# Performance work log

Hardware: AMD Instinct MI355X
Metric: run time of the kernel (lower is better)

The kernel has to match this reference:

```python
import jax, jax.numpy as jnp
import numpy as np

B, T, TB, TV, TR = 4, 512, 512, 512, 256
D, H = 1024, 16
HD = D // H
D4 = D // 4
DFF = 4096
ROPE_THETA = 10000.0


def _rms(x, w, eps=1e-6):
    return x * jax.lax.rsqrt(jnp.mean(x * x, -1, keepdims=True) + eps) * w


def _ln(x, w, b, eps=1e-5):
    m = jnp.mean(x, -1, keepdims=True)
    v = jnp.var(x, -1, keepdims=True)
    return (x - m) * jax.lax.rsqrt(v + eps) * w + b


def _rope_cs(L, hd):
    inv = 1.0 / (ROPE_THETA ** (jnp.arange(0, hd, 2, dtype=jnp.float32) / hd))
    f = jnp.arange(L, dtype=jnp.float32)[:, None] * inv[None, :]
    e = jnp.concatenate([f, f], -1)  # (L, hd)
    return jnp.cos(e), jnp.sin(e)


def _rot_half(x):
    h = x.shape[-1] // 2
    return jnp.concatenate([-x[..., h:], x[..., :h]], -1)


def _rope(x, cos, sin):
    return x * cos + _rot_half(x) * sin


def _heads(x):
    b, l, _ = x.shape
    return x.reshape(b, l, H, HD).transpose(0, 2, 1, 3)  # (B,H,L,hd)


def setup_inputs() -> dict:
    key = jax.random.key(0)
    ks = jax.random.split(key, 16)
    def n(k, shape, s=0.02):
        return jax.random.normal(k, shape, jnp.float32) * s
    return {
        'x': n(ks[0], (B, T, D), 1.0),
        'bev_tokens': n(ks[1], (B, TB, D), 1.0),
        'vl_tokens': n(ks[2], (B, TV, D), 1.0),
        'reasoning_tokens': n(ks[3], (B, TR, D), 1.0),
        'conditioning': n(ks[4], (B, D), 1.0),
        'ln_pre_w': jnp.ones((D,)), 'ln_pre_b': jnp.zeros((D,)),
        'adaln_w': n(ks[5], (6 * D, D)), 'adaln_b': jnp.zeros((6 * D,)),
        'q_proj_w': n(ks[6], (D, D)), 'q_proj_b': jnp.zeros((D,)),
        'qa_w': n(ks[7], (3, D4, D)), 'qa_b': jnp.zeros((3, D4)),
        'qa_out_w': n(ks[8], (D, D4)), 'qa_out_b': jnp.zeros((D,)),
        'k_w': n(ks[9], (4, D, D)), 'k_b': jnp.zeros((4, D)),
        'v_w': n(ks[10], (4, D, D)), 'v_b': jnp.zeros((4, D)),
        'o_w': n(ks[11], (D, D)), 'o_b': jnp.zeros((D,)),
        'qn_w': jnp.ones((HD,)), 'kn_w': jnp.ones((HD,)),
        'gating': jnp.full((1,), 0.5, jnp.float32),
        'temps': jnp.zeros((4,)), 'score_biases': jnp.zeros((4,)),
        'ffn_ln_w': jnp.ones((D,)), 'ffn_ln_b': jnp.zeros((D,)),
        'ffn_w1': n(ks[12], (DFF, D)), 'ffn_b1': jnp.zeros((DFF,)),
        'ffn_w2': n(ks[13], (D, DFF)), 'ffn_b2': jnp.zeros((D,)),
    }


def reference(x, bev_tokens, vl_tokens, reasoning_tokens, conditioning,
              ln_pre_w, ln_pre_b, adaln_w, adaln_b,
              q_proj_w, q_proj_b, qa_w, qa_b, qa_out_w, qa_out_b,
              k_w, k_b, v_w, v_b, o_w, o_b, qn_w, kn_w,
              gating, temps, score_biases,
              ffn_ln_w, ffn_ln_b, ffn_w1, ffn_b1, ffn_w2, ffn_b2):
    # AdaLN modulation (T_route == 0 path: single modulation for whole sequence)
    mod = jax.nn.silu(conditioning) @ adaln_w.T + adaln_b  # (B, 6D)
    shift_pre, scale_pre, gate_attn, shift_ffn, scale_ffn, gate_ffn = jnp.split(mod, 6, axis=1)
    x_norm = _ln(x, ln_pre_w, ln_pre_b) * (1.0 + scale_pre[:, None, :]) + shift_pre[:, None, :]

    # Self Q and per-source K/V (sources: self, bev, vl, reasoning)
    q_self = _heads(x_norm @ q_proj_w.T + q_proj_b)
    srcs = [x_norm, bev_tokens, vl_tokens, reasoning_tokens]
    k_all = [_heads(s @ k_w[i].T + k_b[i]) for i, s in enumerate(srcs)]
    v_all = [_heads(s @ v_w[i].T + v_b[i]) for i, s in enumerate(srcs)]

    # Source-specific adapter queries: d -> d/4 -> d (shared out proj)
    q_ad = [_heads((x_norm @ qa_w[i].T + qa_b[i]) @ qa_out_w.T + qa_out_b) for i in range(3)]

    # QK-Norm (RMSNorm on head_dim)
    q_all = [_rms(q, qn_w) for q in [q_self] + q_ad]
    k_all = [_rms(k, kn_w) for k in k_all]

    # RoPE: Q and K for self-attention; K only for cross sources
    cosT, sinT = _rope_cs(x.shape[1], HD)
    q_all[0] = _rope(q_all[0], cosT, sinT)
    k_roped = []
    for k in k_all:
        c, s = _rope_cs(k.shape[2], HD)
        k_roped.append(_rope(k, c, s))

    # Per-source temperature / bias; gating only on reasoning scores
    temp = 1.0 + jax.nn.softplus(temps)
    ratio_g = jnp.tanh(gating[0])
    inv_sqrt_d = HD ** -0.5
    scores = []
    for i in range(4):
        s = jnp.einsum('bhqd,bhkd->bhqk', q_all[i], k_roped[i]) * (inv_sqrt_d * temp[i]) + score_biases[i]
        if i == 3:
            s = s * ratio_g
        scores.append(s)

    attn = jax.nn.softmax(jnp.concatenate(scores, -1), axis=-1)  # joint softmax
    v_cat = jnp.concatenate(v_all, 2)  # (B,H,T+TB+TV+TR,hd)
    out = jnp.einsum('bhqk,bhkd->bhqd', attn, v_cat)
    out = out.transpose(0, 2, 1, 3).reshape(x.shape) @ o_w.T + o_b
    x = x + gate_attn[:, None, :] * out

    # FFN with AdaLN modulation (dropout = identity at eval)
    h = _ln(x, ffn_ln_w, ffn_ln_b) * (1.0 + scale_ffn[:, None, :]) + shift_ffn[:, None, :]
    h = jax.nn.gelu(h @ ffn_w1.T + ffn_b1, approximate=False) @ ffn_w2.T + ffn_b2
    return x + gate_ffn[:, None, :] * h
```

## Files before the change

### kernel.cpp

```cpp
#include <hip/hip_runtime.h>

typedef unsigned short ushort_t;
typedef __attribute__((ext_vector_type(8))) __bf16 bf16x8;
typedef __attribute__((ext_vector_type(4))) float f32x4;

__device__ __forceinline__ float bf2f(ushort_t u) {
    union { unsigned int i; float f; } v; v.i = ((unsigned int)u) << 16; return v.f;
}
__device__ __forceinline__ ushort_t f2bf(float f) {
    union { float f; unsigned int i; } v; v.f = f;
    unsigned int r = (v.i + 0x7FFFu + ((v.i >> 16) & 1u)) >> 16;
    return (ushort_t)r;
}
__device__ __forceinline__ float gelu_exact(float v) {
    return 0.5f * v * (1.f + erff(v * 0.70710678118654752f));
}
__device__ __forceinline__ float ld1(const void* p, size_t i, int isf32) {
    return isf32 ? ((const float*)p)[i] : bf2f(((const ushort_t*)p)[i]);
}
__device__ __forceinline__ void stage8(const void* p, size_t idx, int isf32, ushort_t* dst) {
    if (isf32) {
        const float* f = (const float*)p + idx;
        float4 u = *(const float4*)f;
        float4 v = *(const float4*)(f + 4);
        dst[0] = f2bf(u.x); dst[1] = f2bf(u.y); dst[2] = f2bf(u.z); dst[3] = f2bf(u.w);
        dst[4] = f2bf(v.x); dst[5] = f2bf(v.y); dst[6] = f2bf(v.z); dst[7] = f2bf(v.w);
    } else {
        *(uint4*)dst = *(const uint4*)((const ushort_t*)p + idx);
    }
}
__device__ __forceinline__ void gload16(const ushort_t* g, ushort_t* l) {
    __builtin_amdgcn_global_load_lds(
        (const __attribute__((address_space(1))) unsigned int*)g,
        (__attribute__((address_space(3))) unsigned int*)l, 16, 0, 0);
}

__device__ __forceinline__ void store_q(ushort_t* qbuf, int row, int c, int p0, float v) {
    int b = row >> 9, t = row & 511;
    qbuf[((((size_t)(b * 16 + (c >> 6))) * 4 + p0) * 512 + t) * 64 + (c & 63)] = f2bf(v);
}
__device__ __forceinline__ void store_k(ushort_t* kbuf, int row, int c, int koff, int p1, float v) {
    int b = row >> p1, t = row & ((1 << p1) - 1);
    kbuf[(((size_t)(b * 16 + (c >> 6))) * 1792 + koff + t) * 64 + (c & 63)] = f2bf(v);
}
__device__ __forceinline__ void store_v(ushort_t* vbufT, int row, int c, int koff, int p1, float v) {
    int b = row >> p1, t = row & ((1 << p1) - 1);
    vbufT[(((size_t)(b * 16 + (c >> 6))) * 64 + (c & 63)) * 1792 + koff + t] = f2bf(v);
}

__global__ void detect_kernel(const unsigned int* __restrict__ x, int* __restrict__ flag) {
    if (threadIdx.x == 0 && blockIdx.x == 0) {
        int sane = 0;
        for (int i = 0; i < 256; i++) {
            unsigned int e = (x[i] >> 7) & 0xFFu;
            if (e == 0u || (e >= 100u && e <= 140u)) sane++;
        }
        *flag = (sane >= 200) ? 0 : 1;
    }
}

static constexpr size_t CW_QPROJ = 0;
static constexpr size_t CW_QA    = 1048576;
static constexpr size_t CW_QAOUT = 1835008;
static constexpr size_t CW_KW    = 2097152;
static constexpr size_t CW_VW    = 6291456;
static constexpr size_t CW_OW    = 10485760;
static constexpr size_t CW_FFN1  = 11534336;
static constexpr size_t CW_FFN2  = 15728640;
static constexpr size_t CW_TOTAL = 19922944;

__global__ void __launch_bounds__(256) convert_weights_kernel(
    const void* s0, const void* s1, const void* s2, const void* s3,
    const void* s4, const void* s5, const void* s6, const void* s7,
    ushort_t* __restrict__ dst, const int* __restrict__ dflag) {
    int isf32 = *dflag;
    size_t i8 = ((size_t)blockIdx.x * 256 + threadIdx.x) * 8;
    if (i8 >= CW_TOTAL) return;
    const void* src; size_t base;
    if      (i8 < CW_QA)    { src = s0; base = CW_QPROJ; }
    else if (i8 < CW_QAOUT) { src = s1; base = CW_QA; }
    else if (i8 < CW_KW)    { src = s2; base = CW_QAOUT; }
    else if (i8 < CW_VW)    { src = s3; base = CW_KW; }
    else if (i8 < CW_OW)    { src = s4; base = CW_VW; }
    else if (i8 < CW_FFN1)  { src = s5; base = CW_OW; }
    else if (i8 < CW_FFN2)  { src = s6; base = CW_FFN1; }
    else                    { src = s7; base = CW_FFN2; }
    ushort_t t8[8];
    stage8(src, i8 - base, isf32, t8);
    *(uint4*)(dst + i8) = *(uint4*)t8;
}

__global__ void __launch_bounds__(256) convert_act3_kernel(
    const void* __restrict__ bev, const void* __restrict__ vl,
    const void* __restrict__ reas, ushort_t* __restrict__ actA,
    ushort_t* __restrict__ actB, const int* __restrict__ dflag) {
    int isf32 = *dflag;
    size_t i8 = ((size_t)blockIdx.x * 256 + threadIdx.x) * 8;
    if (i8 >= 5242880) return;
    ushort_t t8[8];
    if (i8 < 2097152) {
        stage8(bev, i8, isf32, t8);
        *(uint4*)(actA + i8) = *(uint4*)t8;
    } else if (i8 < 4194304) {
        stage8(vl, i8 - 2097152, isf32, t8);
        *(uint4*)(actA + i8) = *(uint4*)t8;
    } else {
        stage8(reas, i8 - 4194304, isf32, t8);
        *(uint4*)(actB + (i8 - 4194304)) = *(uint4*)t8;
    }
}

__global__ void prep_consts_kernel(const void* __restrict__ temps,
                                   const void* __restrict__ biases,
                                   const void* __restrict__ gating,
                                   float* __restrict__ consts,
                                   const int* __restrict__ dflag) {
    if (threadIdx.x == 0 && blockIdx.x == 0) {
        int isf32 = *dflag;
        float g = tanhf(ld1(gating, 0, isf32));
        for (int s = 0; s < 4; s++) {
            float t  = ld1(temps, s, isf32);
            float sp = (t > 20.f) ? t : log1pf(expf(t));
            float scale = 0.125f * (1.f + sp);
            float mul = (s == 3) ? g : 1.f;
            consts[s]     = scale * mul;
            consts[4 + s] = ld1(biases, s, isf32) * mul;
        }
    }
}

__global__ void __launch_bounds__(256) adaln_kernel(
    const void* __restrict__ cond, const void* __restrict__ w,
    const void* __restrict__ bias, float* __restrict__ mod,
    int wmode, const int* __restrict__ dflag) {
    __shared__ float cs[1024];
    int isf32 = *dflag;
    int wf = (wmode == 2) ? 0 : isf32;
    int b = blockIdx.y, tid = threadIdx.x;
    for (int i = tid; i < 1024; i += 256) {
        float c = ld1(cond, b * 1024 + i, isf32);
        cs[i] = c / (1.f + expf(-c));
    }
    __syncthreads();
    int n = blockIdx.x * 256 + tid;
    float acc = 0.f;
    if (wf) {
        const float* wr = (const float*)w + (size_t)n * 1024;
        for (int d = 0; d < 1024; d += 8) {
            float4 a = *(const float4*)(wr + d);
            float4 bb = *(const float4*)(wr + d + 4);
            acc += cs[d+0]*a.x + cs[d+1]*a.y + cs[d+2]*a.z + cs[d+3]*a.w
                 + cs[d+4]*bb.x + cs[d+5]*bb.y + cs[d+6]*bb.z + cs[d+7]*bb.w;
        }
    } else {
        const ushort_t* wr = (const ushort_t*)w + (size_t)n * 1024;
        for (int d = 0; d < 1024; d += 8) {
            uint4 raw = *(const uint4*)(wr + d);
            const ushort_t* u = (const ushort_t*)&raw;
            acc += cs[d+0]*bf2f(u[0]) + cs[d+1]*bf2f(u[1]) + cs[d+2]*bf2f(u[2]) + cs[d+3]*bf2f(u[3])
                 + cs[d+4]*bf2f(u[4]) + cs[d+5]*bf2f(u[5]) + cs[d+6]*bf2f(u[6]) + cs[d+7]*bf2f(u[7]);
        }
    }
    mod[(size_t)b * 6144 + n] = acc + ld1(bias, n, isf32);
}

template <int SRC>
__global__ void __launch_bounds__(256) ln_mod_kernel(
    const void* __restrict__ xin, const float* __restrict__ mod,
    const void* __restrict__ lnw, const void* __restrict__ lnb,
    int shift_off, int scale_off, ushort_t* __restrict__ out,
    const int* __restrict__ dflag) {
    int isf32 = *dflag;
    int row = blockIdx.x, tid = threadIdx.x;
    int b = row >> 9;
    float v[4];
    #pragma unroll
    for (int i = 0; i < 4; i++) {
        size_t idx = (size_t)row * 1024 + tid + 256 * i;
        v[i] = (SRC == 1) ? ((const float*)xin)[idx] : ld1(xin, idx, isf32);
    }
    float s = v[0] + v[1] + v[2] + v[3];
    float ss = v[0]*v[0] + v[1]*v[1] + v[2]*v[2] + v[3]*v[3];
    #pragma unroll
    for (int off = 1; off < 64; off <<= 1) {
        s  += __shfl_xor(s,  off, 64);
        ss += __shfl_xor(ss, off, 64);
    }
    __shared__ float red[8];
    int w = tid >> 6;
    if ((tid & 63) == 0) { red[w] = s; red[4 + w] = ss; }
    __syncthreads();
    s  = red[0] + red[1] + red[2] + red[3];
    ss = red[4] + red[5] + red[6] + red[7];
    float mean = s * (1.f / 1024.f);
    float var  = ss * (1.f / 1024.f) - mean * mean;
    float inv  = rsqrtf(var + 1e-5f);
    const float* mb = mod + (size_t)b * 6144;
    #pragma unroll
    for (int i = 0; i < 4; i++) {
        int d = tid + 256 * i;
        float xn = (v[i] - mean) * inv;
        float y  = xn * ld1(lnw, d, isf32) + ld1(lnb, d, isf32);
        out[(size_t)row * 1024 + d] = f2bf(y * (1.f + mb[scale_off + d]) + mb[shift_off + d]);
    }
}

template <int EPI>
__global__ void __launch_bounds__(256) gemm_bt_kernel(
    const void* __restrict__ A, int lda,
    const void* __restrict__ W, int wrow0,
    const void* __restrict__ bias,
    void* __restrict__ Cout, int ldc, int K, int p0, int p1,
    int a_ext, int wmode, const int* __restrict__ dflag) {
    __shared__ ushort_t As[64][40];
    __shared__ ushort_t Bs[64][40];
    int isf32 = *dflag;
    int fa = a_ext ? isf32 : 0;
    int fw = (wmode == 2) ? 0 : isf32;
    int m0 = blockIdx.x * 64, n0 = blockIdx.y * 64;
    int tid = threadIdx.x;
    int r = tid >> 2, c = (tid & 3) * 8;
    int w = tid >> 6, ln = tid & 63;
    int msub = (w & 1) * 32, nsub = (w >> 1) * 32;
    int fr = ln & 15, q = ln >> 4;
    f32x4 acc00 = {0.f,0.f,0.f,0.f}, acc01 = {0.f,0.f,0.f,0.f};
    f32x4 acc10 = {0.f,0.f,0.f,0.f}, acc11 = {0.f,0.f,0.f,0.f};
    for (int k0 = 0; k0 < K; k0 += 32) {
        __syncthreads();
        {
            ushort_t t8[8];
            stage8(A, (size_t)(m0 + r) * lda + c + k0, fa, t8);
            *(uint4*)&As[r][c] = *(uint4*)t8;
        }
        {
            ushort_t t8[8];
            stage8(W, (size_t)(wrow0 + n0 + r) * K + c + k0, fw, t8);
            *(uint4*)&Bs[r][c] = *(uint4*)t8;
        }
        __syncthreads();
        bf16x8 a0 = *(const bf16x8*)&As[msub + fr][q * 8];
        bf16x8 a1 = *(const bf16x8*)&As[msub + 16 + fr][q * 8];
        bf16x8 b0 = *(const bf16x8*)&Bs[nsub + fr][q * 8];
        bf16x8 b1 = *(const bf16x8*)&Bs[nsub + 16 + fr][q * 8];
        acc00 = __builtin_amdgcn_mfma_f32_16x16x32_bf16(a0, b0, acc00, 0, 0, 0);
        acc01 = __builtin_amdgcn_mfma_f32_16x16x32_bf16(a0, b1, acc01, 0, 0, 0);
        acc10 = __builtin_amdgcn_mfma_f32_16x16x32_bf16(a1, b0, acc10, 0, 0, 0);
        acc11 = __builtin_amdgcn_mfma_f32_16x16x32_bf16(a1, b1, acc11, 0, 0, 0);
    }
    int col0 = n0 + nsub + fr;
    float bv0 = ld1(bias, wrow0 + col0, isf32);
    float bv1 = ld1(bias, wrow0 + col0 + 16, isf32);
    #pragma unroll
    for (int mi = 0; mi < 2; mi++) {
        #pragma unroll
        for (int ni = 0; ni < 2; ni++) {
            f32x4 a = (mi == 0) ? (ni == 0 ? acc00 : acc01) : (ni == 0 ? acc10 : acc11);
            int col = col0 + ni * 16;
            float bb = (ni == 0) ? bv0 : bv1;
            #pragma unroll
            for (int e = 0; e < 4; e++) {
                int rowg = m0 + msub + mi * 16 + q * 4 + e;
                float v = a[e] + bb;
                if (EPI == 2) v = gelu_exact(v);
                if (EPI == 0) {
                    ((float*)Cout)[(size_t)rowg * ldc + col] = v;
                } else if (EPI == 1 || EPI == 2) {
                    ((ushort_t*)Cout)[(size_t)rowg * ldc + col] = f2bf(v);
                } else if (EPI == 3) {
                    store_k((ushort_t*)Cout, rowg, col, p0, p1, v);
                } else if (EPI == 5) {
                    store_v((ushort_t*)Cout, rowg, col, p0, p1, v);
                } else {
                    store_q((ushort_t*)Cout, rowg, col, p0, v);
                }
            }
        }
    }
}

__device__ __forceinline__ void gemm_mainloop(
    const ushort_t* __restrict__ A, int lda,
    const ushort_t* __restrict__ W, int ldw,
    int m0, int wrow0, int kbeg, int klen,
    ushort_t* As, ushort_t* Bs, f32x4 acc[4][4])
{
    const int tid = threadIdx.x;
    const int w = tid >> 6;
    const int ln = tid & 63;
    const int fr = ln & 15, q = ln >> 4;
    const int wm = w & 1, wn = w >> 1;
    const ushort_t* gA = A + (size_t)(m0 + (tid >> 2)) * lda + kbeg + (tid & 3) * 8;
    const ushort_t* gW = W + (size_t)(wrow0 + (tid >> 2)) * ldw + kbeg + (tid & 3) * 8;
    const size_t sA = (size_t)64 * lda;
    const size_t sW = (size_t)64 * ldw;
    ushort_t* lA = As + w * 512;
    ushort_t* lB = Bs + w * 512;
    for (int k = 0; k < klen; k += 32) {
        __syncthreads();
        gload16(gA, lA);
        gload16(gA + sA, lA + 2048);
        gload16(gW, lB);
        gload16(gW + sW, lB + 2048);
        gA += 32; gW += 32;
        __syncthreads();
        bf16x8 af[4], bfr[4];
        #pragma unroll
        for (int mi = 0; mi < 4; mi++)
            af[mi] = *(const bf16x8*)&As[(wm * 64 + mi * 16 + fr) * 32 + q * 8];
        #pragma unroll
        for (int ni = 0; ni < 4; ni++)
            bfr[ni] = *(const bf16x8*)&Bs[(wn * 64 + ni * 16 + fr) * 32 + q * 8];
        #pragma unroll
        for (int mi = 0; mi < 4; mi++)
            #pragma unroll
            for (int ni = 0; ni < 4; ni++)
                acc[mi][ni] = __builtin_amdgcn_mfma_f32_16x16x32_bf16(af[mi], bfr[ni], acc[mi][ni], 0, 0, 0);
    }
}

__global__ void __launch_bounds__(256) gemm_qkvqa_kernel(
    const ushort_t* __restrict__ xnorm,
    const ushort_t* __restrict__ Wq, const ushort_t* __restrict__ Wqa,
    const ushort_t* __restrict__ Wk, const ushort_t* __restrict__ Wv,
    const void* __restrict__ bq, const void* __restrict__ bqa,
    const void* __restrict__ bk, const void* __restrict__ bv,
    ushort_t* __restrict__ qbuf, ushort_t* __restrict__ qah,
    ushort_t* __restrict__ kbuf, ushort_t* __restrict__ vbufT,
    const int* __restrict__ dflag)
{
    __shared__ ushort_t As[4096], Bs[4096];
    int isf32 = *dflag;
    int m0 = blockIdx.x * 128, n0 = blockIdx.y * 128;
    int seg, wrow0;
    const ushort_t* W; const void* bias;
    if (n0 < 1024)      { seg = 0; W = Wq;  bias = bq;  wrow0 = n0; }
    else if (n0 < 1792) { seg = 1; W = Wqa; bias = bqa; wrow0 = n0 - 1024; }
    else if (n0 < 2816) { seg = 2; W = Wk;  bias = bk;  wrow0 = n0 - 1792; }
    else                { seg = 3; W = Wv;  bias = bv;  wrow0 = n0 - 2816; }
    f32x4 acc[4][4];
    #pragma unroll
    for (int i = 0; i < 4; i++)
        #pragma unroll
        for (int j = 0; j < 4; j++) acc[i][j] = (f32x4){0.f, 0.f, 0.f, 0.f};
    gemm_mainloop(xnorm, 1024, W, 1024, m0, wrow0, 0, 1024, As, Bs, acc);
    int tid = threadIdx.x, w = tid >> 6, ln = tid & 63;
    int fr = ln & 15, q = ln >> 4, wm = w & 1, wn = w >> 1;
    #pragma unroll
    for (int ni = 0; ni < 4; ni++) {
        int c = wrow0 + wn * 64 + ni * 16 + fr;
        float bb = ld1(bias, c, isf32);
        #pragma unroll
        for (int mi = 0; mi < 4; mi++) {
            #pragma unroll
            for (int e = 0; e < 4; e++) {
                int row = m0 + wm * 64 + mi * 16 + q * 4 + e;
                float v = acc[mi][ni][e] + bb;
                if (seg == 0)      store_q(qbuf, row, c, 0, v);
                else if (seg == 1) qah[(size_t)row * 768 + c] = f2bf(v);
                else if (seg == 2) store_k(kbuf, row, c, 0, 9, v);
                else               store_v(vbufT, row, c, 0, 9, v);
            }
        }
    }
}

__global__ void __launch_bounds__(256) gemm_kvx_kernel(
    const ushort_t* __restrict__ actA, const ushort_t* __restrict__ actB,
    const ushort_t* __restrict__ Wk1, const ushort_t* __restrict__ Wv1,
    const void* __restrict__ kb_, const void* __restrict__ vb_,
    ushort_t* __restrict__ kbuf, ushort_t* __restrict__ vbufT,
    const int* __restrict__ dflag)
{
    __shared__ ushort_t As[4096], Bs[4096];
    int isf32 = *dflag;
    int mb = blockIdx.x;
    int src, koff, p1, srow0, am0;
    const ushort_t* A;
    if (mb < 16)      { src = 0; A = actA; am0 = mb * 128;        srow0 = mb * 128;        koff = 512;  p1 = 9; }
    else if (mb < 32) { src = 1; A = actA; am0 = mb * 128;        srow0 = (mb - 16) * 128; koff = 1024; p1 = 9; }
    else              { src = 2; A = actB; am0 = (mb - 32) * 128; srow0 = (mb - 32) * 128; koff = 1536; p1 = 8; }
    int n0 = blockIdx.y * 128;
    int isK = (n0 < 1024);
    int wrow0 = isK ? n0 : n0 - 1024;
    const ushort_t* W = (isK ? Wk1 : Wv1) + (size_t)src * 1048576;
    const void* bias = isK ? kb_ : vb_;
    int boff = (src + 1) * 1024;
    f32x4 acc[4][4];
    #pragma unroll
    for (int i = 0; i < 4; i++)
        #pragma unroll
        for (int j = 0; j < 4; j++) acc[i][j] = (f32x4){0.f, 0.f, 0.f, 0.f};
    gemm_mainloop(A, 1024, W, 1024, am0, wrow0, 0, 1024, As, Bs, acc);
    int tid = threadIdx.x, w = tid >> 6, ln = tid & 63;
    int fr = ln & 15, q = ln >> 4, wm = w & 1, wn = w >> 1;
    #pragma unroll
    for (int ni = 0; ni < 4; ni++) {
        int c = wrow0 + wn * 64 + ni * 16 + fr;
        float bb = ld1(bias, boff + c, isf32);
        #pragma unroll
        for (int mi = 0; mi < 4; mi++) {
            #pragma unroll
            for (int e = 0; e < 4; e++) {
                int row = srow0 + wm * 64 + mi * 16 + q * 4 + e;
                float v = acc[mi][ni][e] + bb;
                if (isK) store_k(kbuf, row, c, koff, p1, v);
                else     store_v(vbufT, row, c, koff, p1, v);
            }
        }
    }
}

__global__ void __launch_bounds__(256) gemm_qaout_kernel(
    const ushort_t* __restrict__ qah,
    const ushort_t* __restrict__ W, const void* __restrict__ bias,
    ushort_t* __restrict__ qbuf, const int* __restrict__ dflag)
{
    __shared__ ushort_t As[4096], Bs[4096];
    int isf32 = *dflag;
    int m0 = blockIdx.x * 128, n0 = blockIdx.y * 128;
    int z = blockIdx.z;
    const ushort_t* A = qah + (size_t)z * 256;
    f32x4 acc[4][4];
    #pragma unroll
    for (int i = 0; i < 4; i++)
        #pragma unroll
        for (int j = 0; j < 4; j++) acc[i][j] = (f32x4){0.f, 0.f, 0.f, 0.f};
    gemm_mainloop(A, 768, W, 256, m0, n0, 0, 256, As, Bs, acc);
    int tid = threadIdx.x, w = tid >> 6, ln = tid & 63;
    int fr = ln & 15, q = ln >> 4, wm = w & 1, wn = w >> 1;
    #pragma unroll
    for (int ni = 0; ni < 4; ni++) {
        int c = n0 + wn * 64 + ni * 16 + fr;
        float bb = ld1(bias, c, isf32);
        #pragma unroll
        for (int mi = 0; mi < 4; mi++) {
            #pragma unroll
            for (int e = 0; e < 4; e++) {
                int row = m0 + wm * 64 + mi * 16 + q * 4 + e;
                store_q(qbuf, row, c, 1 + z, acc[mi][ni][e] + bb);
            }
        }
    }
}

template <int EPI>
__global__ void __launch_bounds__(256) gemm_plain_kernel(
    const ushort_t* __restrict__ A, int lda,
    const ushort_t* __restrict__ W, int ldw,
    const void* __restrict__ bias,
    void* __restrict__ o0, void* __restrict__ o1,
    void* __restrict__ o2, void* __restrict__ o3,
    int ldc, int ksub, const int* __restrict__ dflag)
{
    __shared__ ushort_t As[4096], Bs[4096];
    int isf32 = *dflag;
    int m0 = blockIdx.x * 128, n0 = blockIdx.y * 128;
    int z = blockIdx.z;
    void* Cout = (z == 0) ? o0 : (z == 1) ? o1 : (z == 2) ? o2 : o3;
    f32x4 acc[4][4];
    #pragma unroll
    for (int i = 0; i < 4; i++)
        #pragma unroll
        for (int j = 0; j < 4; j++) acc[i][j] = (f32x4){0.f, 0.f, 0.f, 0.f};
    gemm_mainloop(A, lda, W, ldw, m0, n0, z * ksub, ksub, As, Bs, acc);
    int tid = threadIdx.x, w = tid >> 6, ln = tid & 63;
    int fr = ln & 15, q = ln >> 4, wm = w & 1, wn = w >> 1;
    #pragma unroll
    for (int ni = 0; ni < 4; ni++) {
        int c = n0 + wn * 64 + ni * 16 + fr;
        float bb = (z == 0) ? ld1(bias, c, isf32) : 0.f;
        #pragma unroll
        for (int mi = 0; mi < 4; mi++) {
            #pragma unroll
            for (int e = 0; e < 4; e++) {
                int row = m0 + wm * 64 + mi * 16 + q * 4 + e;
                float v = acc[mi][ni][e] + bb;
                if (EPI == 2) {
                    ((ushort_t*)Cout)[(size_t)row * ldc + c] = f2bf(gelu_exact(v));
                } else {
                    ((float*)Cout)[(size_t)row * ldc + c] = v;
                }
            }
        }
    }
}

__global__ void __launch_bounds__(256) qrope_ip_kernel(
    ushort_t* __restrict__ qbuf, const void* __restrict__ qnw,
    const int* __restrict__ dflag) {
    int isf32 = *dflag;
    int w = threadIdx.x >> 6, ln = threadIdx.x & 63;
    int flat = blockIdx.x * 4 + w;
    int t = flat & 511, s = (flat >> 9) & 3;
    ushort_t* p = qbuf + (size_t)flat * 64;
    float x = bf2f(p[ln]);
    float ssum = x * x;
    #pragma unroll
    for (int off = 1; off < 64; off <<= 1) ssum += __shfl_xor(ssum, off, 64);
    float y = x * rsqrtf(ssum * (1.f / 64.f) + 1e-6f) * ld1(qnw, ln, isf32);
    if (s == 0) {
        float ang = (float)t * __expf(-(float)(ln & 31) * (9.210340371976184f / 32.f));
        float cs, sn;
        sincosf(ang, &sn, &cs);
        float other = __shfl_xor(y, 32, 64);
        y = y * cs + ((ln < 32) ? -other : other) * sn;
    }
    p[ln] = f2bf(y);
}

__global__ void __launch_bounds__(256) krope_ip_kernel(
    ushort_t* __restrict__ kbuf, const void* __restrict__ knw,
    const int* __restrict__ dflag) {
    int isf32 = *dflag;
    int w = threadIdx.x >> 6, ln = threadIdx.x & 63;
    int flat = blockIdx.x * 4 + w;
    int j = flat % 1792;
    int t = j & 511;
    ushort_t* p = kbuf + (size_t)flat * 64;
    float x = bf2f(p[ln]);
    float ssum = x * x;
    #pragma unroll
    for (int off = 1; off < 64; off <<= 1) ssum += __shfl_xor(ssum, off, 64);
    float y = x * rsqrtf(ssum * (1.f / 64.f) + 1e-6f) * ld1(knw, ln, isf32);
    float ang = (float)t * __expf(-(float)(ln & 31) * (9.210340371976184f / 32.f));
    float cs, sn;
    sincosf(ang, &sn, &cs);
    float other = __shfl_xor(y, 32, 64);
    y = y * cs + ((ln < 32) ? -other : other) * sn;
    p[ln] = f2bf(y);
}

__global__ void __launch_bounds__(256) attn_mfma_kernel(
    const ushort_t* __restrict__ qbuf, const ushort_t* __restrict__ kbuf,
    const ushort_t* __restrict__ vbufT, const float* __restrict__ consts,
    float* __restrict__ pacc0, float* __restrict__ pacc1,
    float* __restrict__ pml) {
    __shared__ ushort_t ks[64][72];
    __shared__ ushort_t vsT[64][72];
    __shared__ ushort_t ps[4][16][72];
    int id = blockIdx.x;
    int g  = (id & 7) | ((id >> 6) << 3);
    int qx = (id >> 3) & 7;
    int bh = g & 63;
    int z  = g >> 6;
    int tid = threadIdx.x, w = tid >> 6, ln = tid & 63;
    int r0 = qx * 64 + w * 16;
    int m = ln & 15, quad = ln >> 4;
    const int ntile = z ? 12 : 16;
    const int keybase = z * 1024;
    const int s0i = z * 2;

    const ushort_t* qb = qbuf + (size_t)bh * 4 * 512 * 64;
    bf16x8 qA0f = *(const bf16x8*)(qb + ((size_t)(s0i * 512 + r0 + m)) * 64 + quad * 8);
    bf16x8 qA1f = *(const bf16x8*)(qb + ((size_t)(s0i * 512 + r0 + m)) * 64 + 32 + quad * 8);
    bf16x8 qB0f = *(const bf16x8*)(qb + ((size_t)((s0i + 1) * 512 + r0 + m)) * 64 + quad * 8);
    bf16x8 qB1f = *(const bf16x8*)(qb + ((size_t)((s0i + 1) * 512 + r0 + m)) * 64 + 32 + quad * 8);

    const float aA = consts[s0i],     bA = consts[4 + s0i];
    const float aB = consts[s0i + 1], bB = consts[4 + s0i + 1];

    float m_i[4], l_i[4];
    f32x4 acc[4];
    #pragma unroll
    for (int e = 0; e < 4; e++) { m_i[e] = -1e30f; l_i[e] = 0.f; }
    #pragma unroll
    for (int d = 0; d < 4; d++) acc[d] = (f32x4){0.f, 0.f, 0.f, 0.f};

    const ushort_t* kb  = kbuf  + (size_t)bh * 1792 * 64 + (size_t)keybase * 64;
    const ushort_t* vbT = vbufT + (size_t)bh * 64 * 1792 + keybase;
    int skey = tid >> 3, sd = (tid & 7) * 8;
    uint4 kreg0 = *(const uint4*)(kb + (size_t)skey * 64 + sd);
    uint4 kreg1 = *(const uint4*)(kb + (size_t)(skey + 32) * 64 + sd);
    uint4 vreg0 = *(const uint4*)(vbT + (size_t)skey * 1792 + sd);
    uint4 vreg1 = *(const uint4*)(vbT + (size_t)(skey + 32) * 1792 + sd);
    *(uint4*)&ks[skey][sd]       = kreg0;
    *(uint4*)&ks[skey + 32][sd]  = kreg1;
    *(uint4*)&vsT[skey][sd]      = vreg0;
    *(uint4*)&vsT[skey + 32][sd] = vreg1;
    __syncthreads();

    for (int ti = 0; ti < ntile; ti++) {
        const bool pf = (ti + 1 < ntile);
        if (pf) {
            int nx = (ti + 1) * 64;
            kreg0 = *(const uint4*)(kb + (size_t)(nx + skey) * 64 + sd);
            kreg1 = *(const uint4*)(kb + (size_t)(nx + skey + 32) * 64 + sd);
            vreg0 = *(const uint4*)(vbT + (size_t)skey * 1792 + nx + sd);
            vreg1 = *(const uint4*)(vbT + (size_t)(skey + 32) * 1792 + nx + sd);
        }
        int sl = (ti >= 8) ? 1 : 0;
        float a_s = sl ? aB : aA;
        float b_s = sl ? bB : bA;
        bf16x8 qA0 = sl ? qB0f : qA0f;
        bf16x8 qA1 = sl ? qB1f : qA1f;
        f32x4 zero = {0.f, 0.f, 0.f, 0.f};
        bf16x8 k0a = *(const bf16x8*)&ks[m][quad * 8];
        bf16x8 k0b = *(const bf16x8*)&ks[m][32 + quad * 8];
        bf16x8 k1a = *(const bf16x8*)&ks[16 + m][quad * 8];
        bf16x8 k1b = *(const bf16x8*)&ks[16 + m][32 + quad * 8];
        bf16x8 k2a = *(const bf16x8*)&ks[32 + m][quad * 8];
        bf16x8 k2b = *(const bf16x8*)&ks[32 + m][32 + quad * 8];
        bf16x8 k3a = *(const bf16x8*)&ks[48 + m][quad * 8];
        bf16x8 k3b = *(const bf16x8*)&ks[48 + m][32 + quad * 8];
        f32x4 sc0 = __builtin_amdgcn_mfma_f32_16x16x32_bf16(qA0, k0a, zero, 0, 0, 0);
        sc0 = __builtin_amdgcn_mfma_f32_16x16x32_bf16(qA1, k0b, sc0, 0, 0, 0);
        f32x4 sc1 = __builtin_amdgcn_mfma_f32_16x16x32_bf16(qA0, k1a, zero, 0, 0, 0);
        sc1 = __builtin_amdgcn_mfma_f32_16x16x32_bf16(qA1, k1b, sc1, 0, 0, 0);
        f32x4 sc2 = __builtin_amdgcn_mfma_f32_16x16x32_bf16(qA0, k2a, zero, 0, 0, 0);
        sc2 = __builtin_amdgcn_mfma_f32_16x16x32_bf16(qA1, k2b, sc2, 0, 0, 0);
        f32x4 sc3 = __builtin_amdgcn_mfma_f32_16x16x32_bf16(qA0, k3a, zero, 0, 0, 0);
        sc3 = __builtin_amdgcn_mfma_f32_16x16x32_bf16(qA1, k3b, sc3, 0, 0, 0);
        #pragma unroll
        for (int e = 0; e < 4; e++) {
            float s0 = sc0[e] * a_s + b_s;
            float s1 = sc1[e] * a_s + b_s;
            float s2 = sc2[e] * a_s + b_s;
            float s3 = sc3[e] * a_s + b_s;
            float mxe = fmaxf(fmaxf(s0, s1), fmaxf(s2, s3));
            #pragma unroll
            for (int off = 1; off < 16; off <<= 1) mxe = fmaxf(mxe, __shfl_xor(mxe, off, 64));
            if (mxe > m_i[e] + 8.f) {
                float alpha = __expf(m_i[e] - mxe);
                m_i[e] = mxe;
                l_i[e] *= alpha;
                acc[0][e] *= alpha; acc[1][e] *= alpha;
                acc[2][e] *= alpha; acc[3][e] *= alpha;
            }
            float p0 = __expf(s0 - m_i[e]), p1 = __expf(s1 - m_i[e]);
            float p2 = __expf(s2 - m_i[e]), p3 = __expf(s3 - m_i[e]);
            l_i[e] += (p0 + p1) + (p2 + p3);
            int row = quad * 4 + e;
            ps[w][row][m]      = f2bf(p0);
            ps[w][row][m + 16] = f2bf(p1);
            ps[w][row][m + 32] = f2bf(p2);
            ps[w][row][m + 48] = f2bf(p3);
        }
        bf16x8 pA0 = *(const bf16x8*)&ps[w][m][quad * 8];
        bf16x8 pA1 = *(const bf16x8*)&ps[w][m][32 + quad * 8];
        #pragma unroll
        for (int dsub = 0; dsub < 4; dsub++) {
            bf16x8 vB0 = *(const bf16x8*)&vsT[dsub * 16 + m][quad * 8];
            bf16x8 vB1 = *(const bf16x8*)&vsT[dsub * 16 + m][32 + quad * 8];
            acc[dsub] = __builtin_amdgcn_mfma_f32_16x16x32_bf16(pA0, vB0, acc[dsub], 0, 0, 0);
            acc[dsub] = __builtin_amdgcn_mfma_f32_16x16x32_bf16(pA1, vB1, acc[dsub], 0, 0, 0);
        }
        if (pf) {
            __syncthreads();
            *(uint4*)&ks[skey][sd]       = kreg0;
            *(uint4*)&ks[skey + 32][sd]  = kreg1;
            *(uint4*)&vsT[skey][sd]      = vreg0;
            *(uint4*)&vsT[skey + 32][sd] = vreg1;
            __syncthreads();
        }
    }
    #pragma unroll
    for (int e = 0; e < 4; e++) {
        float l = l_i[e];
        #pragma unroll
        for (int off = 1; off < 16; off <<= 1) l += __shfl_xor(l, off, 64);
        l_i[e] = l;
    }
    float* pacc = z ? pacc1 : pacc0;
    #pragma unroll
    for (int e = 0; e < 4; e++) {
        int t = r0 + quad * 4 + e;
        if (m == 0) {
            size_t mi = (((size_t)z * 64 + bh) * 512 + t) * 2;
            pml[mi]     = m_i[e];
            pml[mi + 1] = l_i[e];
        }
        #pragma unroll
        for (int dsub = 0; dsub < 4; dsub++) {
            pacc[((size_t)bh * 512 + t) * 64 + dsub * 16 + m] = acc[dsub][e];
        }
    }
}

__global__ void __launch_bounds__(256) attn_combine_kernel(
    const float* __restrict__ pacc0, const float* __restrict__ pacc1,
    const float* __restrict__ pml, ushort_t* __restrict__ attn_out) {
    int tid = threadIdx.x, w = tid >> 6, ln = tid & 63;
    int idx = blockIdx.x * 4 + w;
    int bh = idx >> 9, t = idx & 511;
    int b = bh >> 4, h = bh & 15;
    size_t r = (size_t)bh * 512 + t;
    float m0 = pml[r * 2],                 l0 = pml[r * 2 + 1];
    float m1 = pml[((size_t)32768 + r) * 2], l1 = pml[((size_t)32768 + r) * 2 + 1];
    float M = fmaxf(m0, m1);
    float w0 = __expf(m0 - M), w1 = __expf(m1 - M);
    float inv = 1.f / (l0 * w0 + l1 * w1);
    float a0 = pacc0[r * 64 + ln];
    float a1 = pacc1[r * 64 + ln];
    attn_out[(((size_t)(b * 512 + t)) * 16 + h) * 64 + ln] = f2bf((a0 * w0 + a1 * w1) * inv);
}

__global__ void __launch_bounds__(256) attn_mfma_legacy_kernel(
    const ushort_t* __restrict__ qbuf, const ushort_t* __restrict__ kbuf,
    const ushort_t* __restrict__ vbufT, const float* __restrict__ consts,
    ushort_t* __restrict__ attn_out) {
    __shared__ ushort_t ks[2][64][72];
    __shared__ ushort_t vsT[2][64][72];
    __shared__ ushort_t ps[4][16][72];
    int bh = blockIdx.y;
    int b = bh >> 4, h = bh & 15;
    int tid = threadIdx.x, w = tid >> 6, ln = tid & 63;
    int r0 = blockIdx.x * 64 + w * 16;
    int m = ln & 15, quad = ln >> 4;
    const ushort_t* qb = qbuf + (size_t)bh * 4 * 512 * 64;
    bf16x8 qf[4][2];
    #pragma unroll
    for (int s = 0; s < 4; s++) {
        qf[s][0] = *(const bf16x8*)(qb + ((size_t)(s * 512 + r0 + m)) * 64 + quad * 8);
        qf[s][1] = *(const bf16x8*)(qb + ((size_t)(s * 512 + r0 + m)) * 64 + 32 + quad * 8);
    }
    float m_i[4], l_i[4];
    f32x4 acc[4];
    #pragma unroll
    for (int e = 0; e < 4; e++) { m_i[e] = -1e30f; l_i[e] = 0.f; }
    #pragma unroll
    for (int d = 0; d < 4; d++) acc[d] = (f32x4){0.f, 0.f, 0.f, 0.f};
    const ushort_t* kb  = kbuf  + (size_t)bh * 1792 * 64;
    const ushort_t* vbT = vbufT + (size_t)bh * 64 * 1792;
    int skey = tid >> 3, sd = (tid & 7) * 8;
    uint4 kreg0 = *(const uint4*)(kb + (size_t)skey * 64 + sd);
    uint4 kreg1 = *(const uint4*)(kb + (size_t)(skey + 32) * 64 + sd);
    uint4 vreg0 = *(const uint4*)(vbT + (size_t)skey * 1792 + sd);
    uint4 vreg1 = *(const uint4*)(vbT + (size_t)(skey + 32) * 1792 + sd);
    *(uint4*)&ks[0][skey][sd]       = kreg0;
    *(uint4*)&ks[0][skey + 32][sd]  = kreg1;
    *(uint4*)&vsT[0][skey][sd]      = vreg0;
    *(uint4*)&vsT[0][skey + 32][sd] = vreg1;
    __syncthreads();
    int tcnt = 0, p = 0;
    #pragma unroll
    for (int s = 0; s < 4; s++) {
        const float a_s = consts[s];
        const float b_s = consts[4 + s];
        const bf16x8 qA0 = qf[s][0];
        const bf16x8 qA1 = qf[s][1];
        const int NT = (s == 3) ? 4 : 8;
        for (int ti = 0; ti < NT; ti++) {
            if (tcnt < 27) {
                int nx = (tcnt + 1) * 64;
                kreg0 = *(const uint4*)(kb + (size_t)(nx + skey) * 64 + sd);
                kreg1 = *(const uint4*)(kb + (size_t)(nx + skey + 32) * 64 + sd);
                vreg0 = *(const uint4*)(vbT + (size_t)skey * 1792 + nx + sd);
                vreg1 = *(const uint4*)(vbT + (size_t)(skey + 32) * 1792 + nx + sd);
            }
            f32x4 zero = {0.f, 0.f, 0.f, 0.f};
            bf16x8 k0a = *(const bf16x8*)&ks[p][m][quad * 8];
            bf16x8 k0b = *(const bf16x8*)&ks[p][m][32 + quad * 8];
            bf16x8 k1a = *(const bf16x8*)&ks[p][16 + m][quad * 8];
            bf16x8 k1b = *(const bf16x8*)&ks[p][16 + m][32 + quad * 8];
            bf16x8 k2a = *(const bf16x8*)&ks[p][32 + m][quad * 8];
            bf16x8 k2b = *(const bf16x8*)&ks[p][32 + m][32 + quad * 8];
            bf16x8 k3a = *(const bf16x8*)&ks[p][48 + m][quad * 8];
            bf16x8 k3b = *(const bf16x8*)&ks[p][48 + m][32 + quad * 8];
            f32x4 sc0 = __builtin_amdgcn_mfma_f32_16x16x32_bf16(qA0, k0a, zero, 0, 0, 0);
            sc0 = __builtin_amdgcn_mfma_f32_16x16x32_bf16(qA1, k0b, sc0, 0, 0, 0);
            f32x4 sc1 = __builtin_amdgcn_mfma_f32_16x16x32_bf16(qA0, k1a, zero, 0, 0, 0);
            sc1 = __builtin_amdgcn_mfma_f32_16x16x32_bf16(qA1, k1b, sc1, 0, 0, 0);
            f32x4 sc2 = __builtin_amdgcn_mfma_f32_16x16x32_bf16(qA0, k2a, zero, 0, 0, 0);
            sc2 = __builtin_amdgcn_mfma_f32_16x16x32_bf16(qA1, k2b, sc2, 0, 0, 0);
            f32x4 sc3 = __builtin_amdgcn_mfma_f32_16x16x32_bf16(qA0, k3a, zero, 0, 0, 0);
            sc3 = __builtin_amdgcn_mfma_f32_16x16x32_bf16(qA1, k3b, sc3, 0, 0, 0);
            #pragma unroll
            for (int e = 0; e < 4; e++) {
                float s0 = sc0[e] * a_s + b_s;
                float s1 = sc1[e] * a_s + b_s;
                float s2 = sc2[e] * a_s + b_s;
                float s3 = sc3[e] * a_s + b_s;
                float mxe = fmaxf(fmaxf(s0, s1), fmaxf(s2, s3));
                #pragma unroll
                for (int off = 1; off < 16; off <<= 1) mxe = fmaxf(mxe, __shfl_xor(mxe, off, 64));
                if (mxe > m_i[e] + 8.f) {
                    float alpha = __expf(m_i[e] - mxe);
                    m_i[e] = mxe;
                    l_i[e] *= alpha;
                    acc[0][e] *= alpha; acc[1][e] *= alpha;
                    acc[2][e] *= alpha; acc[3][e] *= alpha;
                }
                float p0 = __expf(s0 - m_i[e]), p1 = __expf(s1 - m_i[e]);
                float p2 = __expf(s2 - m_i[e]), p3 = __expf(s3 - m_i[e]);
                l_i[e] += (p0 + p1) + (p2 + p3);
                int row = quad * 4 + e;
                ps[w][row][m]      = f2bf(p0);
                ps[w][row][m + 16] = f2bf(p1);
                ps[w][row][m + 32] = f2bf(p2);
                ps[w][row][m + 48] = f2bf(p3);
            }
            bf16x8 pA0 = *(const bf16x8*)&ps[w][m][quad * 8];
            bf16x8 pA1 = *(const bf16x8*)&ps[w][m][32 + quad * 8];
            #pragma unroll
            for (int dsub = 0; dsub < 4; dsub++) {
                bf16x8 vB0 = *(const bf16x8*)&vsT[p][dsub * 16 + m][quad * 8];
                bf16x8 vB1 = *(const bf16x8*)&vsT[p][dsub * 16 + m][32 + quad * 8];
                acc[dsub] = __builtin_amdgcn_mfma_f32_16x16x32_bf16(pA0, vB0, acc[dsub], 0, 0, 0);
                acc[dsub] = __builtin_amdgcn_mfma_f32_16x16x32_bf16(pA1, vB1, acc[dsub], 0, 0, 0);
            }
            if (tcnt < 27) {
                *(uint4*)&ks[1 - p][skey][sd]       = kreg0;
                *(uint4*)&ks[1 - p][skey + 32][sd]  = kreg1;
                *(uint4*)&vsT[1 - p][skey][sd]      = vreg0;
                *(uint4*)&vsT[1 - p][skey + 32][sd] = vreg1;
            }
            __syncthreads();
            p ^= 1;
            tcnt++;
        }
    }
    #pragma unroll
    for (int e = 0; e < 4; e++) {
        float l = l_i[e];
        #pragma unroll
        for (int off = 1; off < 16; off <<= 1) l += __shfl_xor(l, off, 64);
        float invl = 1.f / l;
        int t = r0 + quad * 4 + e;
        #pragma unroll
        for (int dsub = 0; dsub < 4; dsub++) {
            int d = dsub * 16 + m;
            attn_out[(((size_t)(b * 512 + t)) * 16 + h) * 64 + d] = f2bf(acc[dsub][e] * invl);
        }
    }
}

__global__ void resgate_kernel(const void* __restrict__ x, const float* __restrict__ p0,
                               const float* __restrict__ p1, const float* __restrict__ p2,
                               const float* __restrict__ p3,
                               const float* __restrict__ mod, float* __restrict__ x1,
                               int sum4, const int* __restrict__ dflag) {
    int isf32 = *dflag;
    int i = blockIdx.x * 256 + threadIdx.x;
    int b = i >> 19, n = i & 1023;
    float proj = p0[i];
    if (sum4) proj += p1[i] + p2[i] + p3[i];
    x1[i] = ld1(x, i, isf32) + mod[(size_t)b * 6144 + 2048 + n] * proj;
}
__global__ void final_kernel(const float* __restrict__ x1, const float* __restrict__ f0,
                             const float* __restrict__ f1, const float* __restrict__ f2,
                             const float* __restrict__ f3,
                             const float* __restrict__ mod, void* __restrict__ out,
                             int sum4, const int* __restrict__ dflag) {
    int isf32 = *dflag;
    int i = blockIdx.x * 256 + threadIdx.x;
    int b = i >> 19, n = i & 1023;
    float ffn = f0[i];
    if (sum4) ffn += f1[i] + f2[i] + f3[i];
    float val = x1[i] + mod[(size_t)b * 6144 + 5120 + n] * ffn;
    if (isf32) ((float*)out)[i] = val;
    else       ((ushort_t*)out)[i] = f2bf(val);
}

static constexpr size_t OFF_CONSTS   = 0;
static constexpr size_t OFF_FLAG     = 64;
static constexpr size_t OFF_MOD      = 512;
static constexpr size_t OFF_XNORM    = OFF_MOD    + 98304;
static constexpr size_t OFF_QAH      = OFF_XNORM  + 4194304;
static constexpr size_t OFF_KBUF     = OFF_XNORM  + 8388608;
static constexpr size_t OFF_VBUF     = OFF_KBUF   + 14680064;
static constexpr size_t OFF_QBUF     = OFF_VBUF   + 14680064;
static constexpr size_t OFF_ATTNOUT  = OFF_QBUF   + 16777216;
static constexpr size_t OFF_WCACHE   = OFF_ATTNOUT + 4194304;
static constexpr size_t OFF_PACC1    = OFF_WCACHE + CW_TOTAL * 2;
static constexpr size_t OFF_PML      = OFF_PACC1  + 8388608;
static constexpr size_t WS_NEED      = OFF_WCACHE + 52428800;

extern "C" void kernel_launch(void* const* d_in, const int* in_sizes, int n_in,
                              void* d_out, int out_size, void* d_ws, size_t ws_size,
                              hipStream_t stream) {
    (void)in_sizes; (void)n_in; (void)out_size;
    const void* x        = d_in[0];
    const void* bev      = d_in[1];
    const void* vl       = d_in[2];
    const void* reas     = d_in[3];
    const void* cond     = d_in[4];
    const void* ln_pre_w = d_in[5];
    const void* ln_pre_b = d_in[6];
    const void* adaln_w  = d_in[7];
    const void* adaln_b  = d_in[8];
    const void* q_proj_w = d_in[9];
    const void* q_proj_b = d_in[10];
    const void* qa_w     = d_in[11];
    const void* qa_b     = d_in[12];
    const void* qa_out_w = d_in[13];
    const void* qa_out_b = d_in[14];
    const void* k_w      = d_in[15];
    const void* k_b      = d_in[16];
    const void* v_w      = d_in[17];
    const void* v_b      = d_in[18];
    const void* o_w      = d_in[19];
    const void* o_b      = d_in[20];
    const void* qn_w     = d_in[21];
    const void* kn_w     = d_in[22];
    const void* gating   = d_in[23];
    const void* temps    = d_in[24];
    const void* sbias    = d_in[25];
    const void* ffn_ln_w = d_in[26];
    const void* ffn_ln_b = d_in[27];
    const void* ffn_w1   = d_in[28];
    const void* ffn_b1   = d_in[29];
    const void* ffn_w2   = d_in[30];
    const void* ffn_b2   = d_in[31];

    char* ws = (char*)d_ws;
    float*    consts   = (float*)(ws + OFF_CONSTS);
    int*      dflag    = (int*)(ws + OFF_FLAG);
    float*    mod      = (float*)(ws + OFF_MOD);
    ushort_t* xnorm    = (ushort_t*)(ws + OFF_XNORM);
    ushort_t* qah      = (ushort_t*)(ws + OFF_QAH);
    ushort_t* kbuf     = (ushort_t*)(ws + OFF_KBUF);
    ushort_t* vbufT    = (ushort_t*)(ws + OFF_VBUF);
    ushort_t* qbuf     = (ushort_t*)(ws + OFF_QBUF);
    ushort_t* attnout  = (ushort_t*)(ws + OFF_ATTNOUT);
    float*    x1       = (float*)(ws + OFF_XNORM);
    ushort_t* hmid     = (ushort_t*)(ws + OFF_KBUF);
    ushort_t* hin      = (ushort_t*)(ws + OFF_ATTNOUT);
    ushort_t* wc       = (ushort_t*)(ws + OFF_WCACHE);
    float*    pacc0    = (float*)(ws + OFF_XNORM);
    float*    pacc1    = (float*)(ws + OFF_PACC1);
    float*    pml      = (float*)(ws + OFF_PML);
    ushort_t* actA     = (ushort_t*)(ws + OFF_PACC1);
    ushort_t* actB     = (ushort_t*)(ws + OFF_ATTNOUT);
    float*    op0      = (float*)(ws + OFF_KBUF);
    float*    op1      = (float*)(ws + OFF_KBUF + 8388608);
    float*    op2      = (float*)(ws + OFF_KBUF + 16777216);
    float*    op3      = (float*)(ws + OFF_QBUF);
    float*    f0       = (float*)(ws + OFF_QBUF);
    float*    f1       = (float*)(ws + OFF_QBUF + 8388608);
    float*    f2       = (float*)(ws + OFF_KBUF + 16777216);
    float*    f3       = (float*)(ws + OFF_PACC1);

    const bool use_cache = (ws_size >= WS_NEED);

    detect_kernel<<<1, 64, 0, stream>>>((const unsigned int*)x, dflag);
    prep_consts_kernel<<<1, 64, 0, stream>>>(temps, sbias, gating, consts, dflag);

    if (use_cache) {
        convert_weights_kernel<<<9728, 256, 0, stream>>>(
            q_proj_w, qa_w, qa_out_w, k_w, v_w, o_w, ffn_w1, ffn_w2, wc, dflag);
        convert_act3_kernel<<<2560, 256, 0, stream>>>(bev, vl, reas, actA, actB, dflag);
        adaln_kernel<<<dim3(24, 4), 256, 0, stream>>>(cond, adaln_w, adaln_b, mod, 0, dflag);
        ln_mod_kernel<0><<<2048, 256, 0, stream>>>(x, mod, ln_pre_w, ln_pre_b, 0, 1024, xnorm, dflag);

        gemm_qkvqa_kernel<<<dim3(16, 30), 256, 0, stream>>>(
            xnorm, wc + CW_QPROJ, wc + CW_QA, wc + CW_KW, wc + CW_VW,
            q_proj_b, qa_b, k_b, v_b, qbuf, qah, kbuf, vbufT, dflag);
        gemm_qaout_kernel<<<dim3(16, 8, 3), 256, 0, stream>>>(
            qah, wc + CW_QAOUT, qa_out_b, qbuf, dflag);
        gemm_kvx_kernel<<<dim3(40, 16), 256, 0, stream>>>(
            actA, actB, wc + CW_KW + 1048576, wc + CW_VW + 1048576,
            k_b, v_b, kbuf, vbufT, dflag);

        qrope_ip_kernel<<<32768, 256, 0, stream>>>(qbuf, qn_w, dflag);
        krope_ip_kernel<<<28672, 256, 0, stream>>>(kbuf, kn_w, dflag);
        attn_mfma_kernel<<<1024, 256, 0, stream>>>(
            qbuf, kbuf, vbufT, consts, pacc0, pacc1, pml);
        attn_combine_kernel<<<8192, 256, 0, stream>>>(pacc0, pacc1, pml, attnout);

        gemm_plain_kernel<0><<<dim3(16, 8, 4), 256, 0, stream>>>(
            attnout, 1024, wc + CW_OW, 1024, o_b, op0, op1, op2, op3, 1024, 256, dflag);
        resgate_kernel<<<8192, 256, 0, stream>>>(x, op0, op1, op2, op3, mod, x1, 1, dflag);
        ln_mod_kernel<1><<<2048, 256, 0, stream>>>(x1, mod, ffn_ln_w, ffn_ln_b, 3072, 4096, hin, dflag);
        gemm_plain_kernel<2><<<dim3(16, 32, 1), 256, 0, stream>>>(
            hin, 1024, wc + CW_FFN1, 1024, ffn_b1, hmid, nullptr, nullptr, nullptr, 4096, 1024, dflag);
        gemm_plain_kernel<0><<<dim3(16, 8, 4), 256, 0, stream>>>(
            hmid, 4096, wc + CW_FFN2, 4096, ffn_b2, f0, f1, f2, f3, 1024, 1024, dflag);
        final_kernel<<<8192, 256, 0, stream>>>(x1, f0, f1, f2, f3, mod, d_out, 1, dflag);
    } else {
        float* proj0L = (float*)(ws + OFF_QBUF);
        adaln_kernel<<<dim3(24, 4), 256, 0, stream>>>(cond, adaln_w, adaln_b, mod, 0, dflag);
        ln_mod_kernel<0><<<2048, 256, 0, stream>>>(x, mod, ln_pre_w, ln_pre_b, 0, 1024, xnorm, dflag);
        gemm_bt_kernel<4><<<dim3(32, 16), 256, 0, stream>>>(xnorm, 1024, q_proj_w, 0, q_proj_b, qbuf, 0, 1024, 0, 9, 0, 0, dflag);
        {
            const void* srcs[4] = {xnorm, bev, vl, reas};
            const int koffs[4] = {0, 512, 1024, 1536};
            const int p1s[4]   = {9, 9, 9, 8};
            for (int i = 0; i < 4; i++) {
                int aext = (i == 0) ? 0 : 1;
                int gx = (i == 3) ? 16 : 32;
                gemm_bt_kernel<3><<<dim3(gx, 16), 256, 0, stream>>>(
                    srcs[i], 1024, k_w, i * 1024, k_b, kbuf, 0, 1024, koffs[i], p1s[i], aext, 0, dflag);
                gemm_bt_kernel<5><<<dim3(gx, 16), 256, 0, stream>>>(
                    srcs[i], 1024, v_w, i * 1024, v_b, vbufT, 0, 1024, koffs[i], p1s[i], aext, 0, dflag);
            }
        }
        gemm_bt_kernel<1><<<dim3(32, 12), 256, 0, stream>>>(xnorm, 1024, qa_w, 0, qa_b, qah, 768, 1024, 0, 0, 0, 0, dflag);
        for (int i = 0; i < 3; i++)
            gemm_bt_kernel<4><<<dim3(32, 16), 256, 0, stream>>>(qah + i * 256, 768, qa_out_w, 0, qa_out_b,
                                                                qbuf, 0, 256, 1 + i, 9, 0, 0, dflag);
        qrope_ip_kernel<<<32768, 256, 0, stream>>>(qbuf, qn_w, dflag);
        krope_ip_kernel<<<28672, 256, 0, stream>>>(kbuf, kn_w, dflag);
        attn_mfma_legacy_kernel<<<dim3(8, 64), 256, 0, stream>>>(qbuf, kbuf, vbufT, consts, attnout);
        gemm_bt_kernel<0><<<dim3(32, 16), 256, 0, stream>>>(attnout, 1024, o_w, 0, o_b, proj0L, 1024, 1024, 0, 0, 0, 0, dflag);
        resgate_kernel<<<8192, 256, 0, stream>>>(x, proj0L, proj0L, proj0L, proj0L, mod, x1, 0, dflag);
        ln_mod_kernel<1><<<2048, 256, 0, stream>>>(x1, mod, ffn_ln_w, ffn_ln_b, 3072, 4096, hin, dflag);
        gemm_bt_kernel<2><<<dim3(32, 64), 256, 0, stream>>>(hin, 1024, ffn_w1, 0, ffn_b1, hmid, 4096, 1024, 0, 0, 0, 0, dflag);
        gemm_bt_kernel<0><<<dim3(32, 16), 256, 0, stream>>>(hmid, 4096, ffn_w2, 0, ffn_b2, proj0L, 1024, 4096, 0, 0, 0, 0, dflag);
        final_kernel<<<8192, 256, 0, stream>>>(x1, proj0L, proj0L, proj0L, proj0L, mod, d_out, 0, dflag);
    }
}
```

Baseline: 582.4 us.

## Double-buffer GEMM LDS tiles and remap block IDs for XCD locality

The shared GEMM mainloop now double-buffers LDS. The next K-slice is loaded asynchronously into the alternate buffer while MFMAs run on the current one, so there is one barrier per iteration instead of two. Several GEMM kernels also remap blockIdx so that consecutive block ids, which are dispatched round-robin across the 8 XCDs, share the same row tile in each XCD's L2. LDS per block doubles, which can lower occupancy, and the remap assumes the relevant grid dimension is a multiple of 8.

```diff
diff --git a/kernel.cpp b/kernel.cpp
--- a/kernel.cpp
+++ b/kernel.cpp
@@ -46,6 +46,14 @@
 __device__ __forceinline__ void store_v(ushort_t* vbufT, int row, int c, int koff, int p1, float v) {
     int b = row >> p1, t = row & ((1 << p1) - 1);
     vbufT[(((size_t)(b * 16 + (c >> 6))) * 64 + (c & 63)) * 1792 + koff + t] = f2bf(v);
+}
+
+__device__ __forceinline__ void xcd_xy(int X, int& x, int& y) {
+    int id = blockIdx.x + X * blockIdx.y;
+    int yl = id & 7;
+    int rest = id >> 3;
+    x = rest % X;
+    y = (rest / X) * 8 + yl;
 }
 
 __global__ void detect_kernel(const unsigned int* __restrict__ x, int* __restrict__ flag) {
@@ -295,21 +303,47 @@
     const size_t sW = (size_t)64 * ldw;
     ushort_t* lA = As + w * 512;
     ushort_t* lB = Bs + w * 512;
-    for (int k = 0; k < klen; k += 32) {
+    gload16(gA, lA);
+    gload16(gA + sA, lA + 2048);
+    gload16(gW, lB);
+    gload16(gW + sW, lB + 2048);
+    gA += 32; gW += 32;
+    __syncthreads();
+    int cur = 0;
+    for (int k = 32; k < klen; k += 32) {
+        const int nxt = cur ^ 1;
+        gload16(gA, lA + nxt * 4096);
+        gload16(gA + sA, lA + nxt * 4096 + 2048);
+        gload16(gW, lB + nxt * 4096);
+        gload16(gW + sW, lB + nxt * 4096 + 2048);
+        gA += 32; gW += 32;
+        const ushort_t* Ac = As + cur * 4096;
+        const ushort_t* Bc = Bs + cur * 4096;
+        bf16x8 af[4], bfr[4];
+        #pragma unroll
+        for (int mi = 0; mi < 4; mi++)
+            af[mi] = *(const bf16x8*)&Ac[(wm * 64 + mi * 16 + fr) * 32 + q * 8];
+        #pragma unroll
+        for (int ni = 0; ni < 4; ni++)
+            bfr[ni] = *(const bf16x8*)&Bc[(wn * 64 + ni * 16 + fr) * 32 + q * 8];
+        #pragma unroll
+        for (int mi = 0; mi < 4; mi++)
+            #pragma unroll
+            for (int ni = 0; ni < 4; ni++)
+                acc[mi][ni] = __builtin_amdgcn_mfma_f32_16x16x32_bf16(af[mi], bfr[ni], acc[mi][ni], 0, 0, 0);
         __syncthreads();
-        gload16(gA, lA);
-        gload16(gA + sA, lA + 2048);
-        gload16(gW, lB);
-        gload16(gW + sW, lB + 2048);
-        gA += 32; gW += 32;
-        __syncthreads();
+        cur = nxt;
+    }
+    {
+        const ushort_t* Ac = As + cur * 4096;
+        const ushort_t* Bc = Bs + cur * 4096;
         bf16x8 af[4], bfr[4];
         #pragma unroll
         for (int mi = 0; mi < 4; mi++)
-            af[mi] = *(const bf16x8*)&As[(wm * 64 + mi * 16 + fr) * 32 + q * 8];
+            af[mi] = *(const bf16x8*)&Ac[(wm * 64 + mi * 16 + fr) * 32 + q * 8];
         #pragma unroll
         for (int ni = 0; ni < 4; ni++)
-            bfr[ni] = *(const bf16x8*)&Bs[(wn * 64 + ni * 16 + fr) * 32 + q * 8];
+            bfr[ni] = *(const bf16x8*)&Bc[(wn * 64 + ni * 16 + fr) * 32 + q * 8];
         #pragma unroll
         for (int mi = 0; mi < 4; mi++)
             #pragma unroll
@@ -328,7 +362,7 @@
     ushort_t* __restrict__ kbuf, ushort_t* __restrict__ vbufT,
     const int* __restrict__ dflag)
 {
-    __shared__ ushort_t As[4096], Bs[4096];
+    __shared__ ushort_t As[8192], Bs[8192];
     int isf32 = *dflag;
     int m0 = blockIdx.x * 128, n0 = blockIdx.y * 128;
     int seg, wrow0;
@@ -371,15 +405,16 @@
     ushort_t* __restrict__ kbuf, ushort_t* __restrict__ vbufT,
     const int* __restrict__ dflag)
 {
-    __shared__ ushort_t As[4096], Bs[4096];
-    int isf32 = *dflag;
-    int mb = blockIdx.x;
+    __shared__ ushort_t As[8192], Bs[8192];
+    int isf32 = *dflag;
+    int mb, ny;
+    xcd_xy(40, mb, ny);
     int src, koff, p1, srow0, am0;
     const ushort_t* A;
     if (mb < 16)      { src = 0; A = actA; am0 = mb * 128;        srow0 = mb * 128;        koff = 512;  p1 = 9; }
     else if (mb < 32) { src = 1; A = actA; am0 = mb * 128;        srow0 = (mb - 16) * 128; koff = 1024; p1 = 9; }
     else              { src = 2; A = actB; am0 = (mb - 32) * 128; srow0 = (mb - 32) * 128; koff = 1536; p1 = 8; }
-    int n0 = blockIdx.y * 128;
+    int n0 = ny * 128;
     int isK = (n0 < 1024);
     int wrow0 = isK ? n0 : n0 - 1024;
     const ushort_t* W = (isK ? Wk1 : Wv1) + (size_t)src * 1048576;
@@ -415,9 +450,11 @@
     const ushort_t* __restrict__ W, const void* __restrict__ bias,
     ushort_t* __restrict__ qbuf, const int* __restrict__ dflag)
 {
-    __shared__ ushort_t As[4096], Bs[4096];
-    int isf32 = *dflag;
-    int m0 = blockIdx.x * 128, n0 = blockIdx.y * 128;
+    __shared__ ushort_t As[8192], Bs[8192];
+    int isf32 = *dflag;
+    int bx, by;
+    xcd_xy(16, bx, by);
+    int m0 = bx * 128, n0 = by * 128;
     int z = blockIdx.z;
     const ushort_t* A = qah + (size_t)z * 256;
     f32x4 acc[4][4];
@@ -452,9 +489,11 @@
     void* __restrict__ o2, void* __restrict__ o3,
     int ldc, int ksub, const int* __restrict__ dflag)
 {
-    __shared__ ushort_t As[4096], Bs[4096];
-    int isf32 = *dflag;
-    int m0 = blockIdx.x * 128, n0 = blockIdx.y * 128;
+    __shared__ ushort_t As[8192], Bs[8192];
+    int isf32 = *dflag;
+    int bx, by;
+    xcd_xy(gridDim.x, bx, by);
+    int m0 = bx * 128, n0 = by * 128;
     int z = blockIdx.z;
     void* Cout = (z == 0) ? o0 : (z == 1) ? o1 : (z == 2) ? o2 : o3;
     f32x4 acc[4][4];
```

Measured after the change: 596.9 us. 1.02x slower.
